# Performance work log

Measured on AMD Instinct MI355X. Metric: run time of the kernel, lower is better.

## Reference

```python
import jax, jax.numpy as jnp
import numpy as np

N = 50000       # nodes
E = 600000      # edges
F_IN = 500      # num_feature
H = 64          # hidden_dim (ODE state = 2*H)
C = 40          # num_class
T = 1.0         # integration time
STEPS = 4       # RK4 steps (16 ODE function evals)


def setup_inputs() -> dict:
    key = jax.random.key(0)
    ks = jax.random.split(key, 7)
    x = jax.random.normal(ks[0], (N, F_IN), dtype=jnp.float32)
    edge_src = jax.random.randint(ks[1], (E,), 0, N, dtype=jnp.int32)
    edge_dst = jax.random.randint(ks[2], (E,), 0, N, dtype=jnp.int32)
    edge_w = jax.random.uniform(ks[3], (E,), dtype=jnp.float32)
    m1_w = jax.random.normal(ks[4], (F_IN, H), dtype=jnp.float32) / np.sqrt(F_IN).astype(np.float32)
    m1_b = jnp.zeros((H,), jnp.float32)
    alpha_train = jnp.ones((N,), jnp.float32)  # alpha * ones(N) with alpha=1.0
    m2_w = jax.random.normal(ks[5], (H, C), dtype=jnp.float32) / np.sqrt(H).astype(np.float32)
    m2_b = jnp.zeros((C,), jnp.float32)
    return dict(x=x, edge_w=edge_w, m1_w=m1_w, m1_b=m1_b,
                alpha_train=alpha_train, m2_w=m2_w, m2_b=m2_b,
                edge_src=edge_src, edge_dst=edge_dst)


def spmm(edge_src, edge_dst, edge_w, z):
    # A @ z where A[i,j] = sum of edge_w over edges (src=i, dst=j)
    msg = edge_w[:, None] * z[edge_dst]           # [E, 2H]
    return jax.ops.segment_sum(msg, edge_src, num_segments=N)


def reference(x, edge_w, m1_w, m1_b, alpha_train, m2_w, m2_b, edge_src, edge_dst):
    # Encoder (dropout is identity in eval mode)
    h = x @ m1_w + m1_b                           # [N, H]
    h = jnp.concatenate([h, jnp.zeros_like(h)], axis=1)  # [N, 2H]
    x0 = jax.lax.stop_gradient(h)                 # x0 = x.clone().detach()
    alph = jax.nn.sigmoid(alpha_train)[:, None]   # [N, 1]

    def f(z):  # ODE RHS: sigmoid(alpha)*0.5*(A z - z) + x0
        az = spmm(edge_src, edge_dst, edge_w, z)
        return alph * 0.5 * (az - z) + x0

    dt = jnp.float32(T / STEPS)

    def step(z, _):
        k1 = f(z)
        k2 = f(z + 0.5 * dt * k1)
        k3 = f(z + 0.5 * dt * k2)
        k4 = f(z + dt * k3)
        return z + (dt / 6.0) * (k1 + 2.0 * k2 + 2.0 * k3 + k4), None

    z, _ = jax.lax.scan(step, h, None, length=STEPS)
    z = jax.nn.relu(z[:, :H])                     # first half of state
    return z @ m2_w + m2_b                        # [N, C]
```

## Files before the change

kernel.cpp:

```cpp
#include <hip/hip_runtime.h>
#include <hip/hip_fp16.h>

#define N_NODES 50000
#define N_EDGES 600000
#define F_IN    500
#define H_DIM   64
#define C_OUT   40
#define STEPS   4
#define NB_SCAN ((N_NODES + 255) / 256)
#define KTILES  16

using half8 = __attribute__((ext_vector_type(8))) _Float16;
using f32x4 = __attribute__((ext_vector_type(4))) float;

__global__ __launch_bounds__(256) void bfrag_kernel(
    const float* __restrict__ W, __half* __restrict__ bfrag)
{
    int t = blockIdx.x * 256 + threadIdx.x;
    if (t >= KTILES * 4 * 64) return;
    int lane = t & 63;
    int c    = (t >> 6) & 3;
    int kt   = t >> 8;
    int col  = c * 16 + (lane & 15);
    int kb   = kt * 32 + (lane >> 4) * 8;
    union { uint4 u; __half h[8]; } v;
    #pragma unroll
    for (int j = 0; j < 8; ++j) {
        int k = kb + j;
        v.h[j] = (k < F_IN) ? __float2half(W[(size_t)k * H_DIM + col]) : __half(0.f);
    }
    *reinterpret_cast<uint4*>(bfrag + (size_t)t * 8) = v.u;
}

__global__ __launch_bounds__(256) void encoder_kernel(
    const float* __restrict__ x, const __half* __restrict__ bfrag,
    const float* __restrict__ b, __half* __restrict__ x0H,
    float* __restrict__ zF, __half* __restrict__ zH)
{
    __shared__ f32x4 red[2][64][4];

    int wave = threadIdx.x >> 6;
    int lane = threadIdx.x & 63;
    int pair = wave >> 1;
    int half = wave & 1;
    int rowl = lane & 15;
    int kg   = lane >> 4;
    int r0   = blockIdx.x * 32 + pair * 16;

    int gr = r0 + rowl; if (gr >= N_NODES) gr = N_NODES - 1;
    const float* xrow = x + (size_t)gr * F_IN;
    const uint4* bf = reinterpret_cast<const uint4*>(bfrag);

    int ktb = half * 8;

    float4 xv[16];
    #pragma unroll
    for (int ki = 0; ki < 8; ++ki) {
        int k0 = (ktb + ki) * 32 + kg * 8;
        xv[2 * ki]     = make_float4(0.f, 0.f, 0.f, 0.f);
        xv[2 * ki + 1] = make_float4(0.f, 0.f, 0.f, 0.f);
        if (k0 + 4 <= F_IN) xv[2 * ki]     = *reinterpret_cast<const float4*>(xrow + k0);
        if (k0 + 8 <= F_IN) xv[2 * ki + 1] = *reinterpret_cast<const float4*>(xrow + k0 + 4);
    }

    f32x4 acc[4];
    #pragma unroll
    for (int c = 0; c < 4; ++c) acc[c] = (f32x4){0.f, 0.f, 0.f, 0.f};

    #pragma unroll
    for (int ki = 0; ki < 8; ++ki) {
        int kt = ktb + ki;
        float4 xa = xv[2 * ki], xb = xv[2 * ki + 1];
        half8 a;
        a[0] = (_Float16)xa.x; a[1] = (_Float16)xa.y;
        a[2] = (_Float16)xa.z; a[3] = (_Float16)xa.w;
        a[4] = (_Float16)xb.x; a[5] = (_Float16)xb.y;
        a[6] = (_Float16)xb.z; a[7] = (_Float16)xb.w;
        #pragma unroll
        for (int c = 0; c < 4; ++c) {
            union { uint4 u; half8 h; } bv;
            bv.u = bf[(size_t)(kt * 4 + c) * 64 + lane];
            acc[c] = __builtin_amdgcn_mfma_f32_16x16x32_f16(a, bv.h, acc[c], 0, 0, 0);
        }
    }

    if (half == 1) {
        #pragma unroll
        for (int c = 0; c < 4; ++c) red[pair][lane][c] = acc[c];
    }
    __syncthreads();
    if (half == 0) {
        #pragma unroll
        for (int c = 0; c < 4; ++c) {
            f32x4 r = red[pair][lane][c];
            acc[c][0] += r[0]; acc[c][1] += r[1];
            acc[c][2] += r[2]; acc[c][3] += r[3];
        }
        #pragma unroll
        for (int c = 0; c < 4; ++c) {
            int col = c * 16 + rowl;
            float bias = b[col];
            #pragma unroll
            for (int r = 0; r < 4; ++r) {
                int grow = r0 + kg * 4 + r;
                if (grow < N_NODES) {
                    float v = acc[c][r] + bias;
                    size_t idx = (size_t)grow * H_DIM + col;
                    zF[idx]  = v;
                    __half hv = __float2half(v);
                    zH[idx]  = hv;
                    x0H[idx] = hv;
                }
            }
        }
    }
}

__global__ void hist_kernel(const int* __restrict__ src, int* __restrict__ counts)
{
    int e = blockIdx.x * 256 + threadIdx.x;
    if (e < N_EDGES) atomicAdd(&counts[src[e]], 1);
}

__global__ __launch_bounds__(256) void scanA_kernel(
    const int* __restrict__ counts, int* __restrict__ blockSums)
{
    __shared__ int red[256];
    int i = blockIdx.x * 256 + threadIdx.x;
    red[threadIdx.x] = (i < N_NODES) ? counts[i] : 0;
    __syncthreads();
    #pragma unroll
    for (int s = 128; s > 0; s >>= 1) {
        if (threadIdx.x < s) red[threadIdx.x] += red[threadIdx.x + s];
        __syncthreads();
    }
    if (threadIdx.x == 0) blockSums[blockIdx.x] = red[0];
}

__global__ __launch_bounds__(256) void scanB_kernel(
    const int* __restrict__ blockSums, int* __restrict__ blockBases)
{
    __shared__ int s[256];
    int tid = threadIdx.x;
    int v = (tid < NB_SCAN) ? blockSums[tid] : 0;
    s[tid] = v;
    __syncthreads();
    #pragma unroll
    for (int d = 1; d < 256; d <<= 1) {
        int t = (tid >= d) ? s[tid - d] : 0;
        __syncthreads();
        s[tid] += t;
        __syncthreads();
    }
    if (tid < NB_SCAN) blockBases[tid] = s[tid] - v;
}

__global__ __launch_bounds__(256) void scanC_kernel(
    const int* __restrict__ counts, const int* __restrict__ blockBases,
    int* __restrict__ off, int* __restrict__ cursor)
{
    __shared__ int s[256];
    int tid = threadIdx.x;
    int i = blockIdx.x * 256 + tid;
    int v = (i < N_NODES) ? counts[i] : 0;
    s[tid] = v;
    __syncthreads();
    #pragma unroll
    for (int d = 1; d < 256; d <<= 1) {
        int t = (tid >= d) ? s[tid - d] : 0;
        __syncthreads();
        s[tid] += t;
        __syncthreads();
    }
    if (i < N_NODES) {
        int excl = blockBases[blockIdx.x] + s[tid] - v;
        off[i] = excl;
        cursor[i] = excl;
        if (i == N_NODES - 1) off[N_NODES] = excl + v;
    }
}

__global__ void scatter_kernel(const int* __restrict__ src, const int* __restrict__ dst,
                               const float* __restrict__ w,
                               int* __restrict__ cursor, int2* __restrict__ epack)
{
    int e = blockIdx.x * 256 + threadIdx.x;
    if (e < N_EDGES) {
        int s = src[e];
        int p = atomicAdd(&cursor[s], 1);
        epack[p] = make_int2(dst[e], __float_as_int(w[e]));
    }
}

template<int STAGE>
__global__ __launch_bounds__(256) void stage_kernel(
    const int* __restrict__ off, const int2* __restrict__ epack,
    const __half* __restrict__ zsH, const __half* __restrict__ zH,
    const float* __restrict__ zbF, const __half* __restrict__ x0H,
    const float* __restrict__ alpha, __half* __restrict__ accH,
    __half* __restrict__ outH, float* __restrict__ outZ, float cnext)
{
    int node = blockIdx.x * 32 + (threadIdx.x >> 3);
    if (node >= N_NODES) return;
    int c = (threadIdx.x & 7) << 3;

    int jb = off[node], je = off[node + 1];

    union H4 { uint4 u; __half2 h[4]; };

    float azA[8], azB[8];
    #pragma unroll
    for (int i = 0; i < 8; ++i) { azA[i] = 0.f; azB[i] = 0.f; }

#define ACC8(dst, V, W)                                                    \
    {                                                                      \
        float2 f0 = __half22float2((V).h[0]);                              \
        float2 f1 = __half22float2((V).h[1]);                              \
        float2 f2 = __half22float2((V).h[2]);                              \
        float2 f3 = __half22float2((V).h[3]);                              \
        dst[0] = fmaf(W, f0.x, dst[0]); dst[1] = fmaf(W, f0.y, dst[1]);    \
        dst[2] = fmaf(W, f1.x, dst[2]); dst[3] = fmaf(W, f1.y, dst[3]);    \
        dst[4] = fmaf(W, f2.x, dst[4]); dst[5] = fmaf(W, f2.y, dst[5]);    \
        dst[6] = fmaf(W, f3.x, dst[6]); dst[7] = fmaf(W, f3.y, dst[7]);    \
    }

    int j = jb;
    for (; j + 3 < je; j += 4) {
        int2 e0 = epack[j];
        int2 e1 = epack[j + 1];
        int2 e2 = epack[j + 2];
        int2 e3 = epack[j + 3];
        H4 v0, v1, v2, v3;
        v0.u = *reinterpret_cast<const uint4*>(zsH + (size_t)e0.x * H_DIM + c);
        v1.u = *reinterpret_cast<const uint4*>(zsH + (size_t)e1.x * H_DIM + c);
        v2.u = *reinterpret_cast<const uint4*>(zsH + (size_t)e2.x * H_DIM + c);
        v3.u = *reinterpret_cast<const uint4*>(zsH + (size_t)e3.x * H_DIM + c);
        float w0 = __int_as_float(e0.y), w1 = __int_as_float(e1.y);
        float w2 = __int_as_float(e2.y), w3 = __int_as_float(e3.y);
        ACC8(azA, v0, w0);
        ACC8(azB, v1, w1);
        ACC8(azA, v2, w2);
        ACC8(azB, v3, w3);
    }
    for (; j < je; ++j) {
        int2 e0 = epack[j];
        H4 v0;
        v0.u = *reinterpret_cast<const uint4*>(zsH + (size_t)e0.x * H_DIM + c);
        float w0 = __int_as_float(e0.y);
        ACC8(azA, v0, w0);
    }
#undef ACC8

    float az[8];
    #pragma unroll
    for (int i = 0; i < 8; ++i) az[i] = azA[i] + azB[i];

    size_t idx = (size_t)node * H_DIM + c;
    H4 sr; sr.u = *reinterpret_cast<const uint4*>(zsH + idx);
    float s[8];
    {
        float2 f0 = __half22float2(sr.h[0]), f1 = __half22float2(sr.h[1]);
        float2 f2 = __half22float2(sr.h[2]), f3 = __half22float2(sr.h[3]);
        s[0] = f0.x; s[1] = f0.y; s[2] = f1.x; s[3] = f1.y;
        s[4] = f2.x; s[5] = f2.y; s[6] = f3.x; s[7] = f3.y;
    }
    H4 xr; xr.u = *reinterpret_cast<const uint4*>(x0H + idx);
    float xv[8];
    {
        float2 f0 = __half22float2(xr.h[0]), f1 = __half22float2(xr.h[1]);
        float2 f2 = __half22float2(xr.h[2]), f3 = __half22float2(xr.h[3]);
        xv[0] = f0.x; xv[1] = f0.y; xv[2] = f1.x; xv[3] = f1.y;
        xv[4] = f2.x; xv[5] = f2.y; xv[6] = f3.x; xv[7] = f3.y;
    }
    float a = 0.5f / (1.f + __expf(-alpha[node]));

    float k[8];
    #pragma unroll
    for (int i = 0; i < 8; ++i) k[i] = fmaf(a, az[i] - s[i], xv[i]);

    float o[8];
    if constexpr (STAGE == 0) {
        H4 aw;
        aw.h[0] = __float22half2_rn(make_float2(k[0], k[1]));
        aw.h[1] = __float22half2_rn(make_float2(k[2], k[3]));
        aw.h[2] = __float22half2_rn(make_float2(k[4], k[5]));
        aw.h[3] = __float22half2_rn(make_float2(k[6], k[7]));
        *reinterpret_cast<uint4*>(accH + idx) = aw.u;
        #pragma unroll
        for (int i = 0; i < 8; ++i) o[i] = fmaf(cnext, k[i], s[i]);
    } else if constexpr (STAGE == 1 || STAGE == 2) {
        H4 ar; ar.u = *reinterpret_cast<const uint4*>(accH + idx);
        float av[8];
        {
            float2 f0 = __half22float2(ar.h[0]), f1 = __half22float2(ar.h[1]);
            float2 f2 = __half22float2(ar.h[2]), f3 = __half22float2(ar.h[3]);
            av[0] = f0.x; av[1] = f0.y; av[2] = f1.x; av[3] = f1.y;
            av[4] = f2.x; av[5] = f2.y; av[6] = f3.x; av[7] = f3.y;
        }
        #pragma unroll
        for (int i = 0; i < 8; ++i) av[i] = fmaf(2.f, k[i], av[i]);
        H4 aw;
        aw.h[0] = __float22half2_rn(make_float2(av[0], av[1]));
        aw.h[1] = __float22half2_rn(make_float2(av[2], av[3]));
        aw.h[2] = __float22half2_rn(make_float2(av[4], av[5]));
        aw.h[3] = __float22half2_rn(make_float2(av[6], av[7]));
        *reinterpret_cast<uint4*>(accH + idx) = aw.u;
        H4 br; br.u = *reinterpret_cast<const uint4*>(zH + idx);
        float bv[8];
        {
            float2 f0 = __half22float2(br.h[0]), f1 = __half22float2(br.h[1]);
            float2 f2 = __half22float2(br.h[2]), f3 = __half22float2(br.h[3]);
            bv[0] = f0.x; bv[1] = f0.y; bv[2] = f1.x; bv[3] = f1.y;
            bv[4] = f2.x; bv[5] = f2.y; bv[6] = f3.x; bv[7] = f3.y;
        }
        #pragma unroll
        for (int i = 0; i < 8; ++i) o[i] = fmaf(cnext, k[i], bv[i]);
    } else {
        H4 ar; ar.u = *reinterpret_cast<const uint4*>(accH + idx);
        float av[8];
        {
            float2 f0 = __half22float2(ar.h[0]), f1 = __half22float2(ar.h[1]);
            float2 f2 = __half22float2(ar.h[2]), f3 = __half22float2(ar.h[3]);
            av[0] = f0.x; av[1] = f0.y; av[2] = f1.x; av[3] = f1.y;
            av[4] = f2.x; av[5] = f2.y; av[6] = f3.x; av[7] = f3.y;
        }
        float4 zb0 = *reinterpret_cast<const float4*>(zbF + idx);
        float4 zb1 = *reinterpret_cast<const float4*>(zbF + idx + 4);
        float zb[8] = {zb0.x, zb0.y, zb0.z, zb0.w, zb1.x, zb1.y, zb1.z, zb1.w};
        #pragma unroll
        for (int i = 0; i < 8; ++i) o[i] = fmaf(cnext, av[i] + k[i], zb[i]);
        float4 oz0 = make_float4(o[0], o[1], o[2], o[3]);
        float4 oz1 = make_float4(o[4], o[5], o[6], o[7]);
        *reinterpret_cast<float4*>(outZ + idx)     = oz0;
        *reinterpret_cast<float4*>(outZ + idx + 4) = oz1;
    }
    H4 sv;
    sv.h[0] = __float22half2_rn(make_float2(o[0], o[1]));
    sv.h[1] = __float22half2_rn(make_float2(o[2], o[3]));
    sv.h[2] = __float22half2_rn(make_float2(o[4], o[5]));
    sv.h[3] = __float22half2_rn(make_float2(o[6], o[7]));
    *reinterpret_cast<uint4*>(outH + idx) = sv.u;
}

__global__ __launch_bounds__(256) void decoder_kernel(
    const float* __restrict__ z, const float* __restrict__ W2,
    const float* __restrict__ b2, float* __restrict__ out)
{
    __shared__ float zsm[4][H_DIM];
    int lane = threadIdx.x & 63;
    int w    = threadIdx.x >> 6;
    int node = blockIdx.x * 4 + w;
    int ld   = node >= N_NODES ? N_NODES - 1 : node;
    float zv = z[(size_t)ld * H_DIM + lane];
    zsm[w][lane] = zv > 0.f ? zv : 0.f;
    __syncthreads();
    if (node < N_NODES && lane < C_OUT) {
        float acc = b2[lane];
        #pragma unroll
        for (int k = 0; k < H_DIM; ++k)
            acc = fmaf(zsm[w][k], W2[k * C_OUT + lane], acc);
        out[(size_t)node * C_OUT + lane] = acc;
    }
}

extern "C" void kernel_launch(void* const* d_in, const int* in_sizes, int n_in,
                              void* d_out, int out_size, void* d_ws, size_t ws_size,
                              hipStream_t stream)
{
    const float* x     = (const float*)d_in[0];
    const float* ew    = (const float*)d_in[1];
    const float* m1w   = (const float*)d_in[2];
    const float* m1b   = (const float*)d_in[3];
    const float* alpha = (const float*)d_in[4];
    const float* m2w   = (const float*)d_in[5];
    const float* m2b   = (const float*)d_in[6];
    const int*   esrc  = (const int*)d_in[7];
    const int*   edst  = (const int*)d_in[8];
    float* out = (float*)d_out;

    char* ws = (char*)d_ws;
    size_t o = 0;
    auto alloc = [&](size_t bytes) -> void* {
        void* p = ws + o;
        o = (o + bytes + 255) & ~(size_t)255;
        return p;
    };
    float*  z      = (float*)alloc((size_t)N_NODES * H_DIM * 4);
    __half* x0H    = (__half*)alloc((size_t)N_NODES * H_DIM * 2);
    __half* zH     = (__half*)alloc((size_t)N_NODES * H_DIM * 2);
    __half* ztAH   = (__half*)alloc((size_t)N_NODES * H_DIM * 2);
    __half* ztBH   = (__half*)alloc((size_t)N_NODES * H_DIM * 2);
    __half* accH   = (__half*)alloc((size_t)N_NODES * H_DIM * 2);
    __half* bfrag  = (__half*)alloc((size_t)KTILES * 4 * 64 * 8 * 2);
    int*    counts = (int*)alloc((size_t)N_NODES * 4);
    int*    off    = (int*)alloc((size_t)(N_NODES + 1) * 4);
    int*    cursor = (int*)alloc((size_t)N_NODES * 4);
    int*    bsums  = (int*)alloc((size_t)NB_SCAN * 4);
    int*    bbases = (int*)alloc((size_t)NB_SCAN * 4);
    int2*   epack  = (int2*)alloc((size_t)N_EDGES * 8);

    hipMemsetAsync(counts, 0, (size_t)N_NODES * 4, stream);
    hist_kernel<<<(N_EDGES + 255) / 256, 256, 0, stream>>>(esrc, counts);
    scanA_kernel<<<NB_SCAN, 256, 0, stream>>>(counts, bsums);
    scanB_kernel<<<1, 256, 0, stream>>>(bsums, bbases);
    scanC_kernel<<<NB_SCAN, 256, 0, stream>>>(counts, bbases, off, cursor);
    scatter_kernel<<<(N_EDGES + 255) / 256, 256, 0, stream>>>(esrc, edst, ew, cursor, epack);

    bfrag_kernel<<<(KTILES * 4 * 64 + 255) / 256, 256, 0, stream>>>(m1w, bfrag);
    encoder_kernel<<<(N_NODES + 31) / 32, 256, 0, stream>>>(x, bfrag, m1b, x0H, z, zH);

    const float dt = 1.0f / STEPS;
    int sgrid = (N_NODES + 31) / 32;
    for (int step = 0; step < STEPS; ++step) {
        stage_kernel<0><<<sgrid, 256, 0, stream>>>(off, epack, zH,   zH, nullptr, x0H, alpha, accH, ztAH, nullptr, 0.5f * dt);
        stage_kernel<1><<<sgrid, 256, 0, stream>>>(off, epack, ztAH, zH, nullptr, x0H, alpha, accH, ztBH, nullptr, 0.5f * dt);
        stage_kernel<2><<<sgrid, 256, 0, stream>>>(off, epack, ztBH, zH, nullptr, x0H, alpha, accH, ztAH, nullptr, dt);
        stage_kernel<3><<<sgrid, 256, 0, stream>>>(off, epack, ztAH, zH, z,       x0H, alpha, accH, zH,   z,       dt / 6.0f);
    }

    decoder_kernel<<<(N_NODES + 3) / 4, 256, 0, stream>>>(z, m2w, m2b, out);
}
```

Baseline: 393.7 us.

## Sort nodes by degree for balanced SpMM stages and prescale edge indices

Adds a counting-sort pass that buckets nodes by out-degree into a node_order permutation. Each stage kernel now maps its 8-lane groups through this order, so the nodes sharing a wavefront have similar edge counts and spend less time idling in divergent edge loops. The destination index is also stored pre-shifted to a byte offset, which drops a multiply from each gather. In exchange, every node needs an extra indirection load, row-wise memory access loses locality, three small setup kernels are added, and node indices above 2^24 would overflow the shifted value.

Measured after the change: 747.4 us. 89.8% more time.

```diff
diff --git a/kernel.cpp b/kernel.cpp
--- a/kernel.cpp
+++ b/kernel.cpp
@@ -9,6 +9,7 @@
 #define STEPS   4
 #define NB_SCAN ((N_NODES + 255) / 256)
 #define KTILES  16
+#define DBINS   64
 
 using half8 = __attribute__((ext_vector_type(8))) _Float16;
 using f32x4 = __attribute__((ext_vector_type(4))) float;
@@ -188,23 +189,55 @@
     if (e < N_EDGES) {
         int s = src[e];
         int p = atomicAdd(&cursor[s], 1);
-        epack[p] = make_int2(dst[e], __float_as_int(w[e]));
+        epack[p] = make_int2(dst[e] << 7, __float_as_int(w[e]));
+    }
+}
+
+__global__ void degHist_kernel(const int* __restrict__ counts, int* __restrict__ binCnt)
+{
+    int i = blockIdx.x * 256 + threadIdx.x;
+    if (i < N_NODES) {
+        int d = counts[i]; if (d > DBINS - 1) d = DBINS - 1;
+        atomicAdd(&binCnt[d], 1);
+    }
+}
+
+__global__ void degScan_kernel(const int* __restrict__ binCnt, int* __restrict__ binCur)
+{
+    if (threadIdx.x == 0) {
+        int r = 0;
+        for (int d = 0; d < DBINS; ++d) { binCur[d] = r; r += binCnt[d]; }
+    }
+}
+
+__global__ void degScatter_kernel(const int* __restrict__ counts, int* __restrict__ binCur,
+                                  int* __restrict__ node_order)
+{
+    int i = blockIdx.x * 256 + threadIdx.x;
+    if (i < N_NODES) {
+        int d = counts[i]; if (d > DBINS - 1) d = DBINS - 1;
+        int p = atomicAdd(&binCur[d], 1);
+        node_order[p] = i;
     }
 }
 
 template<int STAGE>
 __global__ __launch_bounds__(256) void stage_kernel(
+    const int* __restrict__ node_order,
     const int* __restrict__ off, const int2* __restrict__ epack,
     const __half* __restrict__ zsH, const __half* __restrict__ zH,
     const float* __restrict__ zbF, const __half* __restrict__ x0H,
     const float* __restrict__ alpha, __half* __restrict__ accH,
     __half* __restrict__ outH, float* __restrict__ outZ, float cnext)
 {
-    int node = blockIdx.x * 32 + (threadIdx.x >> 3);
-    if (node >= N_NODES) return;
-    int c = (threadIdx.x & 7) << 3;
+    int nidx = blockIdx.x * 32 + (threadIdx.x >> 3);
+    if (nidx >= N_NODES) return;
+    int node = node_order[nidx];
+    int cb = (threadIdx.x & 7) << 4;
+    int c  = cb >> 1;
 
     int jb = off[node], je = off[node + 1];
+    const char* rdB = reinterpret_cast<const char*>(zsH);
 
     union H4 { uint4 u; __half2 h[4]; };
 
@@ -231,10 +264,10 @@
         int2 e2 = epack[j + 2];
         int2 e3 = epack[j + 3];
         H4 v0, v1, v2, v3;
-        v0.u = *reinterpret_cast<const uint4*>(zsH + (size_t)e0.x * H_DIM + c);
-        v1.u = *reinterpret_cast<const uint4*>(zsH + (size_t)e1.x * H_DIM + c);
-        v2.u = *reinterpret_cast<const uint4*>(zsH + (size_t)e2.x * H_DIM + c);
-        v3.u = *reinterpret_cast<const uint4*>(zsH + (size_t)e3.x * H_DIM + c);
+        v0.u = *reinterpret_cast<const uint4*>(rdB + (size_t)(unsigned)e0.x + cb);
+        v1.u = *reinterpret_cast<const uint4*>(rdB + (size_t)(unsigned)e1.x + cb);
+        v2.u = *reinterpret_cast<const uint4*>(rdB + (size_t)(unsigned)e2.x + cb);
+        v3.u = *reinterpret_cast<const uint4*>(rdB + (size_t)(unsigned)e3.x + cb);
         float w0 = __int_as_float(e0.y), w1 = __int_as_float(e1.y);
         float w2 = __int_as_float(e2.y), w3 = __int_as_float(e3.y);
         ACC8(azA, v0, w0);
@@ -245,7 +278,7 @@
     for (; j < je; ++j) {
         int2 e0 = epack[j];
         H4 v0;
-        v0.u = *reinterpret_cast<const uint4*>(zsH + (size_t)e0.x * H_DIM + c);
+        v0.u = *reinterpret_cast<const uint4*>(rdB + (size_t)(unsigned)e0.x + cb);
         float w0 = __int_as_float(e0.y);
         ACC8(azA, v0, w0);
     }
@@ -397,25 +430,33 @@
     int*    cursor = (int*)alloc((size_t)N_NODES * 4);
     int*    bsums  = (int*)alloc((size_t)NB_SCAN * 4);
     int*    bbases = (int*)alloc((size_t)NB_SCAN * 4);
+    int*    binCnt = (int*)alloc((size_t)DBINS * 4);
+    int*    binCur = (int*)alloc((size_t)DBINS * 4);
+    int*    nodeOrd= (int*)alloc((size_t)N_NODES * 4);
     int2*   epack  = (int2*)alloc((size_t)N_EDGES * 8);
 
     hipMemsetAsync(counts, 0, (size_t)N_NODES * 4, stream);
+    hipMemsetAsync(binCnt, 0, (size_t)DBINS * 4, stream);
     hist_kernel<<<(N_EDGES + 255) / 256, 256, 0, stream>>>(esrc, counts);
     scanA_kernel<<<NB_SCAN, 256, 0, stream>>>(counts, bsums);
     scanB_kernel<<<1, 256, 0, stream>>>(bsums, bbases);
     scanC_kernel<<<NB_SCAN, 256, 0, stream>>>(counts, bbases, off, cursor);
     scatter_kernel<<<(N_EDGES + 255) / 256, 256, 0, stream>>>(esrc, edst, ew, cursor, epack);
 
+    degHist_kernel<<<NB_SCAN, 256, 0, stream>>>(counts, binCnt);
+    degScan_kernel<<<1, 64, 0, stream>>>(binCnt, binCur);
+    degScatter_kernel<<<NB_SCAN, 256, 0, stream>>>(counts, binCur, nodeOrd);
+
     bfrag_kernel<<<(KTILES * 4 * 64 + 255) / 256, 256, 0, stream>>>(m1w, bfrag);
     encoder_kernel<<<(N_NODES + 31) / 32, 256, 0, stream>>>(x, bfrag, m1b, x0H, z, zH);
 
     const float dt = 1.0f / STEPS;
     int sgrid = (N_NODES + 31) / 32;
     for (int step = 0; step < STEPS; ++step) {
-        stage_kernel<0><<<sgrid, 256, 0, stream>>>(off, epack, zH,   zH, nullptr, x0H, alpha, accH, ztAH, nullptr, 0.5f * dt);
-        stage_kernel<1><<<sgrid, 256, 0, stream>>>(off, epack, ztAH, zH, nullptr, x0H, alpha, accH, ztBH, nullptr, 0.5f * dt);
-        stage_kernel<2><<<sgrid, 256, 0, stream>>>(off, epack, ztBH, zH, nullptr, x0H, alpha, accH, ztAH, nullptr, dt);
-        stage_kernel<3><<<sgrid, 256, 0, stream>>>(off, epack, ztAH, zH, z,       x0H, alpha, accH, zH,   z,       dt / 6.0f);
+        stage_kernel<0><<<sgrid, 256, 0, stream>>>(nodeOrd, off, epack, zH,   zH, nullptr, x0H, alpha, accH, ztAH, nullptr, 0.5f * dt);
+        stage_kernel<1><<<sgrid, 256, 0, stream>>>(nodeOrd, off, epack, ztAH, zH, nullptr, x0H, alpha, accH, ztBH, nullptr, 0.5f * dt);
+        stage_kernel<2><<<sgrid, 256, 0, stream>>>(nodeOrd, off, epack, ztBH, zH, nullptr, x0H, alpha, accH, ztAH, nullptr, dt);
+        stage_kernel<3><<<sgrid, 256, 0, stream>>>(nodeOrd, off, epack, ztAH, zH, z,       x0H, alpha, accH, zH,   z,       dt / 6.0f);
     }
 
     decoder_kernel<<<(N_NODES + 3) / 4, 256, 0, stream>>>(z, m2w, m2b, out);
```
